# Kernel tuning notes

Hardware: AMD Instinct MI355X
Metric: run time of the kernel (lower is better)

The kernel has to match this reference:

```python
import jax, jax.numpy as jnp
from jax import lax
import numpy as np

HIDDEN = 128  # ConvLSTM hidden channels


def _conv(x, w, b, stride):
    # torch Conv2d(kernel=3, padding=1), NCHW / OIHW
    y = lax.conv_general_dilated(x, w, stride, [(1, 1), (1, 1)],
                                 dimension_numbers=('NCHW', 'OIHW', 'NCHW'))
    return y + b[None, :, None, None]


def _convT(x, w, b):
    # torch ConvTranspose2d(k=3, stride=(2,1), padding=1, output_padding=(1,0))
    # torch weight layout [Cin, Cout, kH, kW] -> flip spatially, swap IO
    wf = jnp.flip(w, (2, 3)).transpose(1, 0, 2, 3)
    y = lax.conv_general_dilated(x, wf, (1, 1), [(1, 2), (1, 1)],
                                 lhs_dilation=(2, 1),
                                 dimension_numbers=('NCHW', 'OIHW', 'NCHW'))
    return y + b[None, :, None, None]


def _bn(x, g, be, m, v):
    # eval-mode BatchNorm2d, eps=1e-5
    return g[None, :, None, None] * (x - m[None, :, None, None]) * lax.rsqrt(v[None, :, None, None] + 1e-5) + be[None, :, None, None]


def _lrelu(x):
    return jnp.where(x >= 0, x, 0.2 * x)


def _convlstm(e5, w, b):
    # e5: [B, 256, F, T]; scan over time with h,c state of shape [B, HIDDEN, F, 1]
    B, C, F, T = e5.shape
    xs = jnp.moveaxis(e5, 3, 0)[..., None]  # [T, B, C, F, 1]
    h0 = jnp.zeros((B, HIDDEN, F, 1), e5.dtype)

    def step(carry, xt):
        h, c = carry
        gates = _conv(jnp.concatenate([xt, h], axis=1), w, b, (1, 1))  # [B, 4H, F, 1]
        i, f, o, g = jnp.split(gates, 4, axis=1)
        c = jax.nn.sigmoid(f) * c + jax.nn.sigmoid(i) * jnp.tanh(g)
        h = jax.nn.sigmoid(o) * jnp.tanh(c)
        return (h, c), h

    _, hs = lax.scan(step, (h0, h0), xs)  # hs: [T, B, H, F, 1]
    return jnp.moveaxis(hs[..., 0], 0, 3)  # [B, H, F, T]


def _forward(x, enc1_w, enc1_b, enc1_g, enc1_be, enc1_m, enc1_v, enc2_w, enc2_b, enc2_g, enc2_be, enc2_m, enc2_v, enc3_w, enc3_b, enc3_g, enc3_be, enc3_m, enc3_v, enc4_w, enc4_b, enc4_g, enc4_be, enc4_m, enc4_v, enc5_w, enc5_b, enc5_g, enc5_be, enc5_m, enc5_v, lstm_w, lstm_b, dec5_w, dec5_b, dec5_g, dec5_be, dec5_m, dec5_v, dec4_w, dec4_b, dec4_g, dec4_be, dec4_m, dec4_v, dec3_w, dec3_b, dec3_g, dec3_be, dec3_m, dec3_v, dec2_w, dec2_b, dec2_g, dec2_be, dec2_m, dec2_v, dec1_w, dec1_b):
    x_log = jnp.log10(x + 1e-8)
    e1 = _lrelu(_bn(_conv(x_log, enc1_w, enc1_b, (2, 1)), enc1_g, enc1_be, enc1_m, enc1_v))
    e2 = _lrelu(_bn(_conv(e1, enc2_w, enc2_b, (2, 1)), enc2_g, enc2_be, enc2_m, enc2_v))
    e3 = _lrelu(_bn(_conv(e2, enc3_w, enc3_b, (2, 1)), enc3_g, enc3_be, enc3_m, enc3_v))
    e4 = _lrelu(_bn(_conv(e3, enc4_w, enc4_b, (2, 1)), enc4_g, enc4_be, enc4_m, enc4_v))
    e5 = _lrelu(_bn(_conv(e4, enc5_w, enc5_b, (2, 1)), enc5_g, enc5_be, enc5_m, enc5_v))
    lstm_out = _convlstm(e5, lstm_w, lstm_b)  # [B, 128, 8, T]
    d5 = jax.nn.relu(_bn(_convT(lstm_out, dec5_w, dec5_b), dec5_g, dec5_be, dec5_m, dec5_v))
    d4 = jax.nn.relu(_bn(_convT(jnp.concatenate([d5, e4], 1), dec4_w, dec4_b), dec4_g, dec4_be, dec4_m, dec4_v))
    d3 = jax.nn.relu(_bn(_convT(jnp.concatenate([d4, e3], 1), dec3_w, dec3_b), dec3_g, dec3_be, dec3_m, dec3_v))
    d2 = jax.nn.relu(_bn(_convT(jnp.concatenate([d3, e2], 1), dec2_w, dec2_b), dec2_g, dec2_be, dec2_m, dec2_v))
    mask = jax.nn.sigmoid(_convT(jnp.concatenate([d2, e1], 1), dec1_w, dec1_b))
    return x * mask


def setup_inputs() -> dict:
    key = jax.random.key(0)
    ks = list(jax.random.split(key, 64))
    it = iter(ks)
    d = {}
    d['x'] = jax.random.uniform(next(it), (16, 1, 256, 512), jnp.float32)

    def conv_block(name, cin, cout, bn=True):
        d[name + '_w'] = jax.random.normal(next(it), (cout, cin, 3, 3), jnp.float32) * 0.05
        d[name + '_b'] = jnp.zeros((cout,), jnp.float32)
        if bn:
            d[name + '_g'] = jnp.ones((cout,), jnp.float32)
            d[name + '_be'] = jnp.zeros((cout,), jnp.float32)
            d[name + '_m'] = jax.random.normal(next(it), (cout,), jnp.float32) * 0.01
            d[name + '_v'] = jnp.ones((cout,), jnp.float32)

    def convT_block(name, cin, cout, bn=True):
        # torch ConvTranspose2d weight [Cin, Cout, kH, kW]
        d[name + '_w'] = jax.random.normal(next(it), (cin, cout, 3, 3), jnp.float32) * 0.05
        d[name + '_b'] = jnp.zeros((cout,), jnp.float32)
        if bn:
            d[name + '_g'] = jnp.ones((cout,), jnp.float32)
            d[name + '_be'] = jnp.zeros((cout,), jnp.float32)
            d[name + '_m'] = jax.random.normal(next(it), (cout,), jnp.float32) * 0.01
            d[name + '_v'] = jnp.ones((cout,), jnp.float32)

    for i, (ci, co) in enumerate([(1, 16), (16, 32), (32, 64), (64, 128), (128, 256)], start=1):
        conv_block(f'enc{i}', ci, co)
    d['lstm_w'] = jax.random.normal(next(it), (4 * HIDDEN, 256 + HIDDEN, 3, 3), jnp.float32) * 0.05
    d['lstm_b'] = jnp.zeros((4 * HIDDEN,), jnp.float32)
    convT_block('dec5', 128, 128)
    convT_block('dec4', 256, 64)
    convT_block('dec3', 128, 32)
    convT_block('dec2', 64, 16)
    convT_block('dec1', 32, 1, bn=False)
    return d


def reference(x, enc1_w, enc1_b, enc1_g, enc1_be, enc1_m, enc1_v, enc2_w, enc2_b, enc2_g, enc2_be, enc2_m, enc2_v, enc3_w, enc3_b, enc3_g, enc3_be, enc3_m, enc3_v, enc4_w, enc4_b, enc4_g, enc4_be, enc4_m, enc4_v, enc5_w, enc5_b, enc5_g, enc5_be, enc5_m, enc5_v, lstm_w, lstm_b, dec5_w, dec5_b, dec5_g, dec5_be, dec5_m, dec5_v, dec4_w, dec4_b, dec4_g, dec4_be, dec4_m, dec4_v, dec3_w, dec3_b, dec3_g, dec3_be, dec3_m, dec3_v, dec2_w, dec2_b, dec2_g, dec2_be, dec2_m, dec2_v, dec1_w, dec1_b):
    return _forward(x, enc1_w, enc1_b, enc1_g, enc1_be, enc1_m, enc1_v, enc2_w, enc2_b, enc2_g, enc2_be, enc2_m, enc2_v, enc3_w, enc3_b, enc3_g, enc3_be, enc3_m, enc3_v, enc4_w, enc4_b, enc4_g, enc4_be, enc4_m, enc4_v, enc5_w, enc5_b, enc5_g, enc5_be, enc5_m, enc5_v, lstm_w, lstm_b, dec5_w, dec5_b, dec5_g, dec5_be, dec5_m, dec5_v, dec4_w, dec4_b, dec4_g, dec4_be, dec4_m, dec4_v, dec3_w, dec3_b, dec3_g, dec3_be, dec3_m, dec3_v, dec2_w, dec2_b, dec2_g, dec2_be, dec2_m, dec2_v, dec1_w, dec1_b)
```

## Files before the change

kernel.cpp:

```cpp
#include <hip/hip_runtime.h>
#include <math.h>


#define WW 512
#define BB 16
#define TT 512

typedef unsigned short u16;
typedef __attribute__((ext_vector_type(8))) short bf16x8;
typedef __attribute__((ext_vector_type(4))) float f32x4;

__device__ __forceinline__ float sigm_(float x){ return 1.f/(1.f+__expf(-x)); }
__device__ __forceinline__ float tanh_(float x){ return 1.f - 2.f/(1.f+__expf(2.f*x)); }
__device__ __forceinline__ float b2f(u16 u){ return __uint_as_float(((unsigned)u)<<16); }
__device__ __forceinline__ u16 f2b(float f){
  unsigned x = __float_as_uint(f);
  return (u16)((x + 0x7fffu + ((x>>16)&1u)) >> 16);
}

__global__ void k_log10(const float* __restrict__ x, u16* __restrict__ y, int n){
  int i = blockIdx.x*256 + threadIdx.x;
  if (i < n) y[i] = f2b(log10f(x[i] + 1e-8f));
}

__global__ __launch_bounds__(128) void k_conv_enc(
    const u16* __restrict__ in, const float* __restrict__ w,
    const float* __restrict__ bias, const float* __restrict__ bg,
    const float* __restrict__ bb_, const float* __restrict__ bm,
    const float* __restrict__ bv, u16* __restrict__ out,
    int Cin, int Cout, int Hin, int Hout)
{
  int blk = blockIdx.x;
  int ho = blk % Hout; blk /= Hout;
  int co = blk % Cout; int b = blk / Cout;
  int t0 = threadIdx.x*4;
  float a0=0.f,a1=0.f,a2=0.f,a3=0.f;
  const float* wb = w + (size_t)co*Cin*9;
  for (int ci=0; ci<Cin; ++ci){
    const u16* ib = in + (size_t)(b*Cin+ci)*Hin*WW;
    const float* wc = wb + ci*9;
    #pragma unroll
    for (int kh=0; kh<3; ++kh){
      int hi = 2*ho + kh - 1;
      if (hi < 0 || hi >= Hin) continue;
      float w0 = wc[kh*3+0], w1 = wc[kh*3+1], w2 = wc[kh*3+2];
      const u16* row = ib + (size_t)hi*WW + t0;
      ushort4 xc = *(const ushort4*)row;
      float x0=b2f(xc.x), x1=b2f(xc.y), x2=b2f(xc.z), x3=b2f(xc.w);
      float xm = (t0==0)    ? 0.f : b2f(row[-1]);
      float xp = (t0+4>=WW) ? 0.f : b2f(row[4]);
      a0 += w0*xm + w1*x0 + w2*x1;
      a1 += w0*x0 + w1*x1 + w2*x2;
      a2 += w0*x1 + w1*x2 + w2*x3;
      a3 += w0*x2 + w1*x3 + w2*xp;
    }
  }
  float sc = bg[co]*rsqrtf(bv[co]+1e-5f);
  float sh = bb_[co] - bm[co]*sc + bias[co]*sc;
  float r0 = sc*a0+sh, r1 = sc*a1+sh, r2 = sc*a2+sh, r3 = sc*a3+sh;
  r0 = (r0>=0.f)?r0:0.2f*r0; r1 = (r1>=0.f)?r1:0.2f*r1;
  r2 = (r2>=0.f)?r2:0.2f*r2; r3 = (r3>=0.f)?r3:0.2f*r3;
  *(ushort4*)(out + ((size_t)((b*Cout+co)*Hout+ho))*WW + t0) =
      make_ushort4(f2b(r0), f2b(r1), f2b(r2), f2b(r3));
}

__global__ __launch_bounds__(256) void k_prep_enc(
    const float* __restrict__ w, const float* __restrict__ b,
    const float* __restrict__ g, const float* __restrict__ be,
    const float* __restrict__ m, const float* __restrict__ v,
    u16* __restrict__ A, float* __restrict__ bias2, int Cin, int Cout, int KPAD)
{
  int co = blockIdx.x;
  float sc = g[co]*rsqrtf(v[co]+1e-5f);
  if (threadIdx.x == 0) bias2[co] = be[co] - m[co]*sc + b[co]*sc;
  for (int idx = threadIdx.x; idx < 3*KPAD; idx += 256){
    int kw = idx / KPAD, k = idx - kw*KPAD;
    float val = 0.f;
    if (k < Cin*3){ int ci = k/3, kh = k - ci*3; val = w[(((size_t)co*Cin+ci)*3+kh)*3+kw]*sc; }
    A[(size_t)(kw*Cout+co)*KPAD + k] = f2b(val);
  }
}

__global__ __launch_bounds__(256) void k_prep_dec(
    const float* __restrict__ w, const float* __restrict__ b,
    const float* __restrict__ g, const float* __restrict__ be,
    const float* __restrict__ m, const float* __restrict__ v,
    u16* __restrict__ AE, u16* __restrict__ AO, float* __restrict__ bias2,
    int Cin, int Cout)
{
  int co = blockIdx.x;
  float sc = g[co]*rsqrtf(v[co]+1e-5f);
  if (threadIdx.x == 0) bias2[co] = be[co] - m[co]*sc + b[co]*sc;
  for (int idx = threadIdx.x; idx < 3*Cin; idx += 256){
    int kw = idx / Cin, ci = idx - kw*Cin;
    const float* wp = w + ((size_t)ci*Cout + co)*9;
    AE[(size_t)(kw*Cout+co)*Cin + ci]          = f2b(wp[3+kw]*sc);
    AO[((size_t)(kw*Cout+co)*Cin + ci)*2 + 0]  = f2b(wp[6+kw]*sc);
    AO[((size_t)(kw*Cout+co)*Cin + ci)*2 + 1]  = f2b(wp[0+kw]*sc);
  }
}

template<int MT,int NT,int WMW,int WNW,int C1,int C2,int COUT,int HIN,int MODE,int MTL>
__global__ __launch_bounds__(256,2) void k_conv_mfma(
    const u16* __restrict__ inA, const u16* __restrict__ inB,
    const u16* __restrict__ AE, const u16* __restrict__ AO,
    const float* __restrict__ bias2, u16* __restrict__ out)
{
  constexpr int CIN  = C1 + C2;
  constexpr int HOUT = MODE ? HIN*2 : HIN/2;
  constexpr int KPAD0 = MODE ? CIN : ((C1*3+31)/32)*32;
  constexpr int LDK = 40;
  __shared__ __align__(16) u16 sB[130*LDK];
  int bi = blockIdx.x;
  int tt = bi & 3; bi >>= 2;
  int mt0 = 0;
  if (MTL == 2){ mt0 = bi & 1; bi >>= 1; }
  int ho = bi % HOUT, b = bi / HOUT;
  int t0 = tt*128;
  int tid = threadIdx.x;
  int w = tid>>6, L = tid&63, q = L>>4, n = L&15;
  int wm = w / WNW, wn = w % WNW;
  int co_base = (mt0*WMW + wm)*MT*16;
  int no = wn*NT*16;
  int odd = MODE ? (ho & 1) : 0;
  int nch     = MODE ? (odd ? CIN/16 : CIN/32) : KPAD0/32;
  int kstride = MODE ? (odd ? 2*CIN : CIN) : KPAD0;
  const u16* Ap = (MODE && odd) ? AO : AE;
  int kloc = tid>>3, seg = tid&7;
  f32x4 cfr[MT][NT];
  #pragma unroll
  for (int mt=0; mt<MT; ++mt)
    #pragma unroll
    for (int nt=0; nt<NT; ++nt){ cfr[mt][nt][0]=0.f; cfr[mt][nt][1]=0.f; cfr[mt][nt][2]=0.f; cfr[mt][nt][3]=0.f; }

  for (int kk=0; kk<nch; ++kk){
    int k = kk*32 + kloc;
    const u16* src = nullptr;
    if (MODE == 0){
      int ci = k/3, kh = k - 3*ci;
      int hi = 2*ho + kh - 1;
      if (k < C1*3 && hi >= 0 && hi < HIN)
        src = inA + ((size_t)(b*C1+ci)*HIN + hi)*WW;
    } else {
      int ci, hi;
      if (!odd){ ci = k; hi = ho>>1; }
      else { ci = k>>1; hi = (k&1) ? ((ho+1)>>1) : ((ho-1)>>1); }
      if (hi < HIN)
        src = (ci < C1) ? inA + ((size_t)(b*C1+ci)*HIN + hi)*WW
                        : inB + ((size_t)(b*C2+(ci-C1))*HIN + hi)*WW;
    }
    uint4 va = make_uint4(0,0,0,0), vb = make_uint4(0,0,0,0);
    u16 hl = 0, hr = 0;
    if (src){
      const u16* p = src + t0 + seg*16;
      va = *(const uint4*)p; vb = *(const uint4*)(p+8);
      if (seg==0 && t0 > 0)      hl = src[t0-1];
      if (seg==1 && t0+128 < WW) hr = src[t0+128];
    }
    __syncthreads();
    {
      const u16* s = (const u16*)&va;
      #pragma unroll
      for (int c=0;c<8;++c) sB[(1+seg*16+c)*LDK + kloc] = s[c];
      s = (const u16*)&vb;
      #pragma unroll
      for (int c=0;c<8;++c) sB[(9+seg*16+c)*LDK + kloc] = s[c];
      if (seg==0) sB[0*LDK + kloc]   = hl;
      if (seg==1) sB[129*LDK + kloc] = hr;
    }
    __syncthreads();
    #pragma unroll
    for (int kw=0; kw<3; ++kw){
      int tsh = MODE ? (2-kw) : kw;
      bf16x8 bfr[NT];
      #pragma unroll
      for (int nt=0; nt<NT; ++nt)
        bfr[nt] = *(const bf16x8*)(sB + (size_t)(no + nt*16 + n + tsh)*LDK + q*8);
      #pragma unroll
      for (int mt=0; mt<MT; ++mt){
        bf16x8 a = *(const bf16x8*)(Ap + ((size_t)(kw*COUT) + co_base + mt*16 + n)*kstride + kk*32 + q*8);
        #pragma unroll
        for (int nt=0; nt<NT; ++nt)
          cfr[mt][nt] = __builtin_amdgcn_mfma_f32_16x16x32_bf16(a, bfr[nt], cfr[mt][nt], 0,0,0);
      }
    }
  }
  #pragma unroll
  for (int mt=0; mt<MT; ++mt){
    #pragma unroll
    for (int r=0; r<4; ++r){
      int co = co_base + mt*16 + q*4 + r;
      float bs = bias2[co];
      #pragma unroll
      for (int nt=0; nt<NT; ++nt){
        float vv = cfr[mt][nt][r] + bs;
        vv = MODE ? fmaxf(vv, 0.f) : ((vv>=0.f)?vv:0.2f*vv);
        int t = t0 + no + nt*16 + n;
        out[((size_t)(b*COUT+co)*HOUT + ho)*WW + t] = f2b(vv);
      }
    }
  }
}

__global__ __launch_bounds__(256) void k_prep_w(
    const float* __restrict__ lstm_w, u16* __restrict__ Wxb, u16* __restrict__ Whb)
{
  int co = blockIdx.x;
  for (int k = threadIdx.x; k < 1152; k += 256){
    if (k < 768){
      int ci = k/3, kf = k - ci*3;
      Wxb[(size_t)co*768 + k] = f2b(lstm_w[((size_t)co*384 + ci)*9 + kf*3 + 1]);
    } else {
      int kh = k - 768;
      int ci = kh/3, kf = kh - ci*3;
      Whb[(size_t)co*384 + kh] = f2b(lstm_w[((size_t)co*384 + 256 + ci)*9 + kf*3 + 1]);
    }
  }
}

__global__ __launch_bounds__(256,3) void k_xconv_mfma(
    const u16* __restrict__ e5, const u16* __restrict__ Wxb,
    const float* __restrict__ bias, u16* __restrict__ gt)
{
  __shared__ __align__(16) u16 smem[128*136];
  int bi = blockIdx.x;
  int tt = bi & 3, cot = (bi>>2) & 3, f = (bi>>4) & 7, b = bi>>7;
  int tid = threadIdx.x, w = tid>>6, L = tid&63, q = L>>4, n = L&15;
  int co_off = (w>>1)*64, t_off = (w&1)*64;
  int sr = tid>>3, sseg = tid&7;
  f32x4 cfr[4][4];
  #pragma unroll
  for (int i=0;i<4;++i)
    #pragma unroll
    for (int j=0;j<4;++j){ cfr[i][j][0]=0.f; cfr[i][j][1]=0.f; cfr[i][j][2]=0.f; cfr[i][j][3]=0.f; }
  const u16* e5b = e5 + (size_t)b*256*8*WW + tt*128 + sseg*16;
  const u16* ap0 = Wxb + (size_t)(cot*128 + co_off + n)*768 + q*8;

  for (int kk=0; kk<24; ++kk){
    int k0 = kk*32;
    {
      int k = k0 + sr;
      int ci = k/3, kf = k - ci*3, fi = f + kf - 1;
      union { uint4 v[2]; u16 s[16]; } uu;
      if (fi >= 0 && fi < 8){
        const u16* src = e5b + ((size_t)ci*8 + fi)*WW;
        uu.v[0] = *(const uint4*)src;
        uu.v[1] = *(const uint4*)(src+8);
      } else {
        uu.v[0] = make_uint4(0,0,0,0); uu.v[1] = make_uint4(0,0,0,0);
      }
      #pragma unroll
      for (int c=0;c<16;++c) smem[(sseg*16+c)*40 + sr] = uu.s[c];
    }
    __syncthreads();
    bf16x8 bfr[4];
    #pragma unroll
    for (int nt=0; nt<4; ++nt)
      bfr[nt] = *(const bf16x8*)(smem + (size_t)(t_off + nt*16 + n)*40 + q*8);
    #pragma unroll
    for (int mt=0; mt<4; ++mt){
      bf16x8 a = *(const bf16x8*)(ap0 + (size_t)mt*16*768 + k0);
      #pragma unroll
      for (int nt=0; nt<4; ++nt)
        cfr[mt][nt] = __builtin_amdgcn_mfma_f32_16x16x32_bf16(a, bfr[nt], cfr[mt][nt], 0,0,0);
    }
    __syncthreads();
  }
  #pragma unroll
  for (int mt=0; mt<4; ++mt){
    #pragma unroll
    for (int r2=0; r2<2; ++r2){
      int co_l = co_off + mt*16 + q*4 + r2*2;
      float bs0 = bias[cot*128 + co_l], bs1 = bias[cot*128 + co_l + 1];
      #pragma unroll
      for (int nt=0; nt<4; ++nt){
        int t_l = t_off + nt*16 + n;
        float v0 = cfr[mt][nt][r2*2]   + bs0;
        float v1 = cfr[mt][nt][r2*2+1] + bs1;
        unsigned pk = (unsigned)f2b(v0) | ((unsigned)f2b(v1)<<16);
        *(unsigned*)(smem + (size_t)t_l*136 + co_l) = pk;
      }
    }
  }
  __syncthreads();
  int row0 = tid>>6, lane2 = tid&63;
  size_t gbase = (((size_t)b*512 + tt*128)*8 + f)*512 + cot*128;
  for (int p=0; p<32; ++p){
    int t_l = p*4 + row0;
    unsigned v = *(const unsigned*)(smem + (size_t)t_l*136 + lane2*2);
    *(unsigned*)(gt + gbase + (size_t)t_l*8*512 + lane2*2) = v;
  }
}

__global__ __launch_bounds__(512,2) void k_lstm_scan(
    const u16* __restrict__ gt, const u16* __restrict__ Whb,
    u16* __restrict__ hs)
{
  __shared__ __align__(16) u16 Bl[6144];
  __shared__ float Gl[512*9];
  int b = blockIdx.x;
  int tid = threadIdx.x, w = tid>>6, L = tid&63, q = L>>4, n = L&15;
  int f2 = tid>>7, ch = tid&127;
  for (int i = tid; i < 6144; i += 512) Bl[i] = 0;
  bf16x8 afr[48];
  #pragma unroll
  for (int mt=0; mt<4; ++mt){
    const u16* ap = Whb + (size_t)(w*64 + mt*16 + n)*384 + q*8;
    #pragma unroll
    for (int kt=0; kt<12; ++kt)
      afr[mt*12+kt] = *(const bf16x8*)(ap + kt*32);
  }
  float c0 = 0.f, c1 = 0.f;
  __syncthreads();
  const size_t gbase = (size_t)b*512;
  for (int t=0; t<TT; ++t){
    const u16* gx = gt + (gbase + t)*4096;
    int fa = f2*2, fb = f2*2+1;
    u16 gi0 = gx[fa*512 +        ch], gi1 = gx[fb*512 +        ch];
    u16 gf0 = gx[fa*512 + 128 + ch], gf1 = gx[fb*512 + 128 + ch];
    u16 go0 = gx[fa*512 + 256 + ch], go1 = gx[fb*512 + 256 + ch];
    u16 gg0 = gx[fa*512 + 384 + ch], gg1 = gx[fb*512 + 384 + ch];
    f32x4 cfr[4];
    #pragma unroll
    for (int mt=0; mt<4; ++mt){ cfr[mt][0]=0.f; cfr[mt][1]=0.f; cfr[mt][2]=0.f; cfr[mt][3]=0.f; }
    #pragma unroll
    for (int kt=0; kt<12; ++kt){
      bf16x8 bfr = *(const bf16x8*)(Bl + ((kt*4+q)*16 + n)*8);
      #pragma unroll
      for (int mt=0; mt<4; ++mt)
        cfr[mt] = __builtin_amdgcn_mfma_f32_16x16x32_bf16(afr[mt*12+kt], bfr, cfr[mt], 0,0,0);
    }
    if (n < 8){
      #pragma unroll
      for (int mt=0; mt<4; ++mt){
        int co = w*64 + mt*16 + q*4;
        #pragma unroll
        for (int r=0; r<4; ++r) Gl[(co+r)*9 + n] = cfr[mt][r];
      }
    }
    __syncthreads();
    float i0 = Gl[ ch      *9 + fa] + b2f(gi0);
    float f0 = Gl[(128+ch)*9 + fa] + b2f(gf0);
    float o0 = Gl[(256+ch)*9 + fa] + b2f(go0);
    float g0 = Gl[(384+ch)*9 + fa] + b2f(gg0);
    float i1 = Gl[ ch      *9 + fb] + b2f(gi1);
    float f1 = Gl[(128+ch)*9 + fb] + b2f(gf1);
    float o1 = Gl[(256+ch)*9 + fb] + b2f(go1);
    float g1 = Gl[(384+ch)*9 + fb] + b2f(gg1);
    c0 = sigm_(f0)*c0 + sigm_(i0)*tanh_(g0);
    c1 = sigm_(f1)*c1 + sigm_(i1)*tanh_(g1);
    float h0 = sigm_(o0)*tanh_(c0);
    float h1 = sigm_(o1)*tanh_(c1);
    u16 hb0 = f2b(h0), hb1 = f2b(h1);
    *(ushort2*)(hs + ((gbase + t)*128 + ch)*8 + fa) = make_ushort2(hb0, hb1);
    #pragma unroll
    for (int i=0; i<2; ++i){
      int fi = f2*2 + i;
      u16 hb = i ? hb1 : hb0;
      #pragma unroll
      for (int kf=0; kf<3; ++kf){
        int ff = fi + 1 - kf;
        if (ff >= 0 && ff < 8){
          int k = ch*3 + kf;
          Bl[((k>>5)*4 + ((k>>3)&3))*128 + ff*8 + (k&7)] = hb;
        }
      }
    }
    __syncthreads();
  }
}

__global__ __launch_bounds__(256) void k_transpose_u16(
    const u16* __restrict__ in, u16* __restrict__ out, int R, int C)
{
  __shared__ u16 tile[32][33];
  int b = blockIdx.z;
  const u16* ip = in  + (size_t)b*R*C;
  u16*       op = out + (size_t)b*R*C;
  int c0 = blockIdx.x*32, r0 = blockIdx.y*32;
  #pragma unroll
  for (int i = threadIdx.y; i < 32; i += 8)
    tile[i][threadIdx.x] = ip[(size_t)(r0+i)*C + (c0+threadIdx.x)];
  __syncthreads();
  #pragma unroll
  for (int i = threadIdx.y; i < 32; i += 8)
    op[(size_t)(c0+i)*R + (r0+threadIdx.x)] = tile[threadIdx.x][i];
}

__global__ __launch_bounds__(128) void k_convT(
    const u16* __restrict__ inA, int C1,
    const u16* __restrict__ inB, int C2,
    const float* __restrict__ w, const float* __restrict__ bias,
    const float* __restrict__ xorig, float* __restrict__ fout,
    int Cout, int Hin)
{
  int Hout = Hin*2;
  int blk = blockIdx.x;
  int y = blk % Hout; blk /= Hout;
  int co = blk % Cout; int b = blk / Cout;
  int t0 = threadIdx.x*4;
  int Cin = C1 + C2;
  int kh0, hi0, kh1 = -1, hi1 = 0;
  if ((y&1)==0){ kh0 = 1; hi0 = y>>1; }
  else { kh0 = 2; hi0 = (y-1)>>1; int h1 = (y+1)>>1; if (h1 < Hin){ kh1 = 0; hi1 = h1; } }
  float a0=0.f,a1=0.f,a2=0.f,a3=0.f;
  for (int ci=0; ci<Cin; ++ci){
    const u16* ib = (ci<C1) ? inA + (size_t)(b*C1+ci)*Hin*WW
                            : inB + (size_t)(b*C2+(ci-C1))*Hin*WW;
    const float* wc = w + ((size_t)ci*Cout + co)*9;
    {
      float w0 = wc[kh0*3+0], w1 = wc[kh0*3+1], w2 = wc[kh0*3+2];
      const u16* row = ib + (size_t)hi0*WW + t0;
      ushort4 xc = *(const ushort4*)row;
      float x0=b2f(xc.x), x1=b2f(xc.y), x2=b2f(xc.z), x3=b2f(xc.w);
      float xm = (t0==0)    ? 0.f : b2f(row[-1]);
      float xp = (t0+4>=WW) ? 0.f : b2f(row[4]);
      a0 += w2*xm + w1*x0 + w0*x1;
      a1 += w2*x0 + w1*x1 + w0*x2;
      a2 += w2*x1 + w1*x2 + w0*x3;
      a3 += w2*x2 + w1*x3 + w0*xp;
    }
    if (kh1 >= 0){
      float w0 = wc[0], w1 = wc[1], w2 = wc[2];
      const u16* row = ib + (size_t)hi1*WW + t0;
      ushort4 xc = *(const ushort4*)row;
      float x0=b2f(xc.x), x1=b2f(xc.y), x2=b2f(xc.z), x3=b2f(xc.w);
      float xm = (t0==0)    ? 0.f : b2f(row[-1]);
      float xp = (t0+4>=WW) ? 0.f : b2f(row[4]);
      a0 += w2*xm + w1*x0 + w0*x1;
      a1 += w2*x0 + w1*x1 + w0*x2;
      a2 += w2*x1 + w1*x2 + w0*x3;
      a3 += w2*x2 + w1*x3 + w0*xp;
    }
  }
  size_t opos = ((size_t)((b*Cout+co)*Hout + y))*WW + t0;
  float bi = bias[co];
  const float4 xv = *(const float4*)(xorig + ((size_t)(b*256 + y))*WW + t0);
  float4 o;
  o.x = xv.x * sigm_(a0+bi); o.y = xv.y * sigm_(a1+bi);
  o.z = xv.z * sigm_(a2+bi); o.w = xv.w * sigm_(a3+bi);
  *(float4*)(fout + opos) = o;
}

extern "C" void kernel_launch(void* const* d_in, const int* in_sizes, int n_in,
                              void* d_out, int out_size, void* d_ws, size_t ws_size,
                              hipStream_t stream) {
  const float* x = (const float*)d_in[0];
  struct Blk { const float *w,*b,*g,*be,*m,*v; };
  auto grab = [&](int p){ return Blk{ (const float*)d_in[p], (const float*)d_in[p+1],
                                      (const float*)d_in[p+2], (const float*)d_in[p+3],
                                      (const float*)d_in[p+4], (const float*)d_in[p+5] }; };
  Blk enc1 = grab(1), enc2 = grab(7), enc3 = grab(13), enc4 = grab(19), enc5 = grab(25);
  const float* lstm_w = (const float*)d_in[31];
  const float* lstm_b = (const float*)d_in[32];
  Blk dec5 = grab(33), dec4 = grab(39), dec3 = grab(45), dec2 = grab(51);
  const float* dec1_w = (const float*)d_in[57];
  const float* dec1_b = (const float*)d_in[58];

  char* ws = (char*)d_ws;
  #define MBOF(x) ((size_t)(x)*1048576ULL)
  u16*   xlog = (u16*)  (ws + MBOF(0));
  u16*   Wxb  = (u16*)  (ws + MBOF(0));
  u16*   Whb  = (u16*)  (ws + MBOF(1));
  char*  P0   =          ws + 1572864;
  u16*   e1   = (u16*)  (ws + MBOF(4));
  u16*   e2   = (u16*)  (ws + MBOF(36));
  u16*   e3   = (u16*)  (ws + MBOF(68));
  u16*   e4   = (u16*)  (ws + MBOF(100));
  u16*   e5   = (u16*)  (ws + MBOF(132));
  u16*   hst  = (u16*)  (ws + MBOF(132));
  u16*   lout = (u16*)  (ws + MBOF(148));
  u16*   gt   = (u16*)  (ws + MBOF(164));
  u16*   d5   = (u16*)  (ws + MBOF(164));
  u16*   d4   = (u16*)  (ws + MBOF(132));
  u16*   d3   = (u16*)  (ws + MBOF(196));
  u16*   d2   = (u16*)  (ws + MBOF(164));

  u16* encA2 = (u16*)(P0 + 0);       u16* encA3 = (u16*)(P0 + 12288);
  u16* encA4 = (u16*)(P0 + 49152);   u16* encA5 = (u16*)(P0 + 196608);
  u16* decE5 = (u16*)(P0 + 786432);  u16* decO5 = (u16*)(P0 + 884736);
  u16* decE4 = (u16*)(P0 + 1081344); u16* decO4 = (u16*)(P0 + 1179648);
  u16* decE3 = (u16*)(P0 + 1376256); u16* decO3 = (u16*)(P0 + 1400832);
  u16* decE2 = (u16*)(P0 + 1449984); u16* decO2 = (u16*)(P0 + 1456128);
  float* bE2 = (float*)(P0 + 1468416); float* bE3 = (float*)(P0 + 1469440);
  float* bE4 = (float*)(P0 + 1470464); float* bE5 = (float*)(P0 + 1471488);
  float* bD5 = (float*)(P0 + 1472512); float* bD4 = (float*)(P0 + 1473536);
  float* bD3 = (float*)(P0 + 1474560); float* bD2 = (float*)(P0 + 1475584);

  { int n = BB*256*WW; k_log10<<<(n+255)/256, 256, 0, stream>>>(x, xlog, n); }
  k_conv_enc<<<BB*16*128, 128, 0, stream>>>(xlog, enc1.w, enc1.b, enc1.g, enc1.be, enc1.m, enc1.v, e1, 1, 16, 256, 128);
  k_prep_w<<<512, 256, 0, stream>>>(lstm_w, Wxb, Whb);
  k_prep_enc<<<32,  256, 0, stream>>>(enc2.w, enc2.b, enc2.g, enc2.be, enc2.m, enc2.v, encA2, bE2, 16, 32, 64);
  k_prep_enc<<<64,  256, 0, stream>>>(enc3.w, enc3.b, enc3.g, enc3.be, enc3.m, enc3.v, encA3, bE3, 32, 64, 96);
  k_prep_enc<<<128, 256, 0, stream>>>(enc4.w, enc4.b, enc4.g, enc4.be, enc4.m, enc4.v, encA4, bE4, 64, 128, 192);
  k_prep_enc<<<256, 256, 0, stream>>>(enc5.w, enc5.b, enc5.g, enc5.be, enc5.m, enc5.v, encA5, bE5, 128, 256, 384);
  k_prep_dec<<<128, 256, 0, stream>>>(dec5.w, dec5.b, dec5.g, dec5.be, dec5.m, dec5.v, decE5, decO5, bD5, 128, 128);
  k_prep_dec<<<64,  256, 0, stream>>>(dec4.w, dec4.b, dec4.g, dec4.be, dec4.m, dec4.v, decE4, decO4, bD4, 256, 64);
  k_prep_dec<<<32,  256, 0, stream>>>(dec3.w, dec3.b, dec3.g, dec3.be, dec3.m, dec3.v, decE3, decO3, bD3, 128, 32);
  k_prep_dec<<<16,  256, 0, stream>>>(dec2.w, dec2.b, dec2.g, dec2.be, dec2.m, dec2.v, decE2, decO2, bD2, 64, 16);
  k_conv_mfma<2,2,1,4, 16,0, 32,128,0,1><<<BB*64*4,   256, 0, stream>>>(e1, e1, encA2, encA2, bE2, e2);
  k_conv_mfma<4,2,1,4, 32,0, 64, 64,0,1><<<BB*32*4,   256, 0, stream>>>(e2, e2, encA3, encA3, bE3, e3);
  k_conv_mfma<4,4,2,2, 64,0,128, 32,0,1><<<BB*16*4,   256, 0, stream>>>(e3, e3, encA4, encA4, bE4, e4);
  k_conv_mfma<4,4,2,2,128,0,256, 16,0,2><<<BB*8*2*4,  256, 0, stream>>>(e4, e4, encA5, encA5, bE5, e5);
  k_xconv_mfma<<<BB*8*16, 256, 0, stream>>>(e5, Wxb, lstm_b, gt);
  k_lstm_scan<<<BB, 512, 0, stream>>>(gt, Whb, hst);
  k_transpose_u16<<<dim3(1024/32, 512/32, BB), dim3(32,8), 0, stream>>>(hst, lout, 512, 1024);
  k_conv_mfma<4,4,2,2,128,  0,128,  8,1,1><<<BB*16*4,  256, 0, stream>>>(lout, lout, decE5, decO5, bD5, d5);
  k_conv_mfma<4,2,1,4,128,128, 64, 16,1,1><<<BB*32*4,  256, 0, stream>>>(d5, e4, decE4, decO4, bD4, d4);
  k_conv_mfma<2,2,1,4, 64, 64, 32, 32,1,1><<<BB*64*4,  256, 0, stream>>>(d4, e3, decE3, decO3, bD3, d3);
  k_conv_mfma<1,2,1,4, 32, 32, 16, 64,1,1><<<BB*128*4, 256, 0, stream>>>(d3, e2, decE2, decO2, bD2, d2);
  k_convT<<<BB*1*256, 128, 0, stream>>>(d2, 16, e1, 16, dec1_w, dec1_b, x, (float*)d_out, 1, 128);
}
```

Baseline: 2.072 ms.

## Prefetch LSTM input gates, remap scan threads, and stagger LDS stores

The ConvLSTM scan kernel now prefetches the next timestep's input-gate values into registers while the current step runs, hiding global load latency on the serial recurrence. Its thread-to-(channel,frequency) mapping is changed and the h scatter addresses into the LDS B-operand buffer are precomputed once, with invalid taps sent to a dummy padding region so the stores need no branches. In the conv and input-projection kernels, the smem transposing stores are rotated by segment to reduce bank conflicts. The input-projection loop's barrier is moved ahead of the smem write instead of after the MFMAs. This costs extra registers and changes how the hs stores coalesce.

```diff
diff --git a/kernel.cpp b/kernel.cpp
--- a/kernel.cpp
+++ b/kernel.cpp
@@ -161,10 +161,10 @@
     {
       const u16* s = (const u16*)&va;
       #pragma unroll
-      for (int c=0;c<8;++c) sB[(1+seg*16+c)*LDK + kloc] = s[c];
+      for (int c=0;c<8;++c){ int vv=(c+seg)&7; sB[(1+seg*16+vv)*LDK + kloc] = s[vv]; }
       s = (const u16*)&vb;
       #pragma unroll
-      for (int c=0;c<8;++c) sB[(9+seg*16+c)*LDK + kloc] = s[c];
+      for (int c=0;c<8;++c){ int vv=(c+seg)&7; sB[(9+seg*16+vv)*LDK + kloc] = s[vv]; }
       if (seg==0) sB[0*LDK + kloc]   = hl;
       if (seg==1) sB[129*LDK + kloc] = hr;
     }
@@ -249,8 +249,9 @@
       } else {
         uu.v[0] = make_uint4(0,0,0,0); uu.v[1] = make_uint4(0,0,0,0);
       }
-      #pragma unroll
-      for (int c=0;c<16;++c) smem[(sseg*16+c)*40 + sr] = uu.s[c];
+      __syncthreads();
+      #pragma unroll
+      for (int c=0;c<16;++c){ int vv=(c+sseg)&15; smem[(sseg*16+vv)*40 + sr] = uu.s[vv]; }
     }
     __syncthreads();
     bf16x8 bfr[4];
@@ -264,8 +265,8 @@
       for (int nt=0; nt<4; ++nt)
         cfr[mt][nt] = __builtin_amdgcn_mfma_f32_16x16x32_bf16(a, bfr[nt], cfr[mt][nt], 0,0,0);
     }
-    __syncthreads();
-  }
+  }
+  __syncthreads();
   #pragma unroll
   for (int mt=0; mt<4; ++mt){
     #pragma unroll
@@ -296,12 +297,12 @@
     const u16* __restrict__ gt, const u16* __restrict__ Whb,
     u16* __restrict__ hs)
 {
-  __shared__ __align__(16) u16 Bl[6144];
+  __shared__ __align__(16) u16 Bl[6144+16];
   __shared__ float Gl[512*9];
   int b = blockIdx.x;
   int tid = threadIdx.x, w = tid>>6, L = tid&63, q = L>>4, n = L&15;
-  int f2 = tid>>7, ch = tid&127;
-  for (int i = tid; i < 6144; i += 512) Bl[i] = 0;
+  int ch = tid>>2, fa = tid&3, fb = fa|4;
+  for (int i = tid; i < 6144+16; i += 512) Bl[i] = 0;
   bf16x8 afr[48];
   #pragma unroll
   for (int mt=0; mt<4; ++mt){
@@ -309,17 +310,37 @@
     #pragma unroll
     for (int kt=0; kt<12; ++kt)
       afr[mt*12+kt] = *(const bf16x8*)(ap + kt*32);
+  }
+  int sa[6];
+  #pragma unroll
+  for (int i2=0;i2<2;++i2){
+    int fi = i2 ? fb : fa;
+    #pragma unroll
+    for (int kf=0;kf<3;++kf){
+      int ff = fi + 1 - kf;
+      int k = ch*3 + kf;
+      sa[i2*3+kf] = (ff>=0 && ff<8)
+          ? (((k>>5)*4 + ((k>>3)&3))*128 + ff*8 + (k&7))
+          : (6144 + (tid&7));
+    }
   }
   float c0 = 0.f, c1 = 0.f;
   __syncthreads();
   const size_t gbase = (size_t)b*512;
+  const u16* pa = gt + gbase*4096 + fa*512 + ch;
+  const u16* pb = gt + gbase*4096 + fb*512 + ch;
+  u16 gc[8];
+  #pragma unroll
+  for (int g=0; g<4; ++g){ gc[g] = pa[g*128]; gc[4+g] = pb[g*128]; }
   for (int t=0; t<TT; ++t){
-    const u16* gx = gt + (gbase + t)*4096;
-    int fa = f2*2, fb = f2*2+1;
-    u16 gi0 = gx[fa*512 +        ch], gi1 = gx[fb*512 +        ch];
-    u16 gf0 = gx[fa*512 + 128 + ch], gf1 = gx[fb*512 + 128 + ch];
-    u16 go0 = gx[fa*512 + 256 + ch], go1 = gx[fb*512 + 256 + ch];
-    u16 gg0 = gx[fa*512 + 384 + ch], gg1 = gx[fb*512 + 384 + ch];
+    u16 gn[8];
+    {
+      int tc = (t+1 < TT) ? (t+1) : t;
+      const u16* qa = pa + (size_t)tc*4096;
+      const u16* qb = pb + (size_t)tc*4096;
+      #pragma unroll
+      for (int g=0; g<4; ++g){ gn[g] = qa[g*128]; gn[4+g] = qb[g*128]; }
+    }
     f32x4 cfr[4];
     #pragma unroll
     for (int mt=0; mt<4; ++mt){ cfr[mt][0]=0.f; cfr[mt][1]=0.f; cfr[mt][2]=0.f; cfr[mt][3]=0.f; }
@@ -339,34 +360,27 @@
       }
     }
     __syncthreads();
-    float i0 = Gl[ ch      *9 + fa] + b2f(gi0);
-    float f0 = Gl[(128+ch)*9 + fa] + b2f(gf0);
-    float o0 = Gl[(256+ch)*9 + fa] + b2f(go0);
-    float g0 = Gl[(384+ch)*9 + fa] + b2f(gg0);
-    float i1 = Gl[ ch      *9 + fb] + b2f(gi1);
-    float f1 = Gl[(128+ch)*9 + fb] + b2f(gf1);
-    float o1 = Gl[(256+ch)*9 + fb] + b2f(go1);
-    float g1 = Gl[(384+ch)*9 + fb] + b2f(gg1);
+    float i0 = Gl[ ch      *9 + fa] + b2f(gc[0]);
+    float f0 = Gl[(128+ch)*9 + fa] + b2f(gc[1]);
+    float o0 = Gl[(256+ch)*9 + fa] + b2f(gc[2]);
+    float g0 = Gl[(384+ch)*9 + fa] + b2f(gc[3]);
+    float i1 = Gl[ ch      *9 + fb] + b2f(gc[4]);
+    float f1 = Gl[(128+ch)*9 + fb] + b2f(gc[5]);
+    float o1 = Gl[(256+ch)*9 + fb] + b2f(gc[6]);
+    float g1 = Gl[(384+ch)*9 + fb] + b2f(gc[7]);
     c0 = sigm_(f0)*c0 + sigm_(i0)*tanh_(g0);
     c1 = sigm_(f1)*c1 + sigm_(i1)*tanh_(g1);
     float h0 = sigm_(o0)*tanh_(c0);
     float h1 = sigm_(o1)*tanh_(c1);
     u16 hb0 = f2b(h0), hb1 = f2b(h1);
-    *(ushort2*)(hs + ((gbase + t)*128 + ch)*8 + fa) = make_ushort2(hb0, hb1);
-    #pragma unroll
-    for (int i=0; i<2; ++i){
-      int fi = f2*2 + i;
-      u16 hb = i ? hb1 : hb0;
-      #pragma unroll
-      for (int kf=0; kf<3; ++kf){
-        int ff = fi + 1 - kf;
-        if (ff >= 0 && ff < 8){
-          int k = ch*3 + kf;
-          Bl[((k>>5)*4 + ((k>>3)&3))*128 + ff*8 + (k&7)] = hb;
-        }
-      }
-    }
+    u16* op = hs + ((gbase + t)*128 + ch)*8;
+    op[fa] = hb0;
+    op[fb] = hb1;
+    Bl[sa[0]] = hb0; Bl[sa[1]] = hb0; Bl[sa[2]] = hb0;
+    Bl[sa[3]] = hb1; Bl[sa[4]] = hb1; Bl[sa[5]] = hb1;
     __syncthreads();
+    #pragma unroll
+    for (int g=0; g<8; ++g) gc[g] = gn[g];
   }
 }
 
```

New measurement: 2.351 ms. +13.5%, slower.
